# Kernel optimization log

Measured on AMD Instinct MI355X. Metric: run time of the kernel, lower is better.

The kernel has to match this reference:

```python
import jax, jax.numpy as jnp
import numpy as np

B, S, D = 2, 2048, 1024
H = 16
HD = D // H  # 64


def setup_inputs() -> dict:
    key = jax.random.key(0)
    k = jax.random.split(key, 6)
    s = 0.02
    return {
        "x": jax.random.normal(k[0], (B, S, D), dtype=jnp.float32),
        "wq": jax.random.normal(k[1], (D, D), dtype=jnp.float32) * s,
        "wk": jax.random.normal(k[2], (D, D), dtype=jnp.float32) * s,
        "wv": jax.random.normal(k[3], (D, D), dtype=jnp.float32) * s,
        "wo": jax.random.normal(k[4], (D, D), dtype=jnp.float32) * s,
        "bo": jnp.zeros((D,), dtype=jnp.float32),
    }


def reference(x, wq, wk, wv, wo, bo):
    b, n, d = x.shape
    # nn.Linear: y = x @ W.T (qkv_bias=False)
    def proj(w):
        y = jnp.einsum('bnd,od->bno', x, w)
        return y.reshape(b, n, H, HD).transpose(0, 2, 1, 3)  # (b, H, n, hd)
    q, k, v = proj(wq), proj(wk), proj(wv)
    scores = jnp.einsum('bhqd,bhkd->bhqk', q, k) / jnp.sqrt(jnp.float32(HD))
    # NOTE: source code slices the causal mask but never applies it; softmax is unmasked.
    attn = jax.nn.softmax(scores, axis=-1)
    # dropout p=0.0 -> identity
    ctx = jnp.einsum('bhqk,bhkd->bhqd', attn, v)
    ctx = ctx.transpose(0, 2, 1, 3).reshape(b, n, d)
    return jnp.einsum('bnd,od->bno', ctx, wo) + bo
```

## Files before the change

### kernel.cpp

```cpp
#include <hip/hip_runtime.h>
#include <hip/hip_bf16.h>
#include <stdint.h>

typedef __attribute__((ext_vector_type(8))) short short8;
typedef __attribute__((ext_vector_type(4))) float float4v;
typedef __attribute__((ext_vector_type(4))) unsigned short ushort4v;

#define Bq 2
#define Sq 2048
#define Dq 1024
#define Hq 16
#define HDq 64

#define QSCALE 0.18033688011112042f

__device__ __forceinline__ unsigned short f2bf(float f) {
  union { float f; uint32_t u; } v; v.f = f;
  uint32_t r = (v.u + 0x7FFFu + ((v.u >> 16) & 1u)) >> 16;
  return (unsigned short)r;
}

__device__ __forceinline__ uint32_t pk2bf(float a, float b) {
  union { __hip_bfloat162 h; uint32_t u; } cv;
  cv.h = __float22bfloat162_rn(make_float2(a, b));
  return cv.u;
}

__device__ __forceinline__ void gl_lds16(const unsigned short* g, unsigned short* l) {
  __builtin_amdgcn_global_load_lds(
      (const __attribute__((address_space(1))) void*)g,
      (__attribute__((address_space(3))) void*)l, 16, 0, 0);
}

__global__ __launch_bounds__(256) void cvt_all_kernel(
    const float* __restrict__ x,
    const float* __restrict__ w0, const float* __restrict__ w1,
    const float* __restrict__ w2, const float* __restrict__ w3,
    unsigned short* __restrict__ xb, unsigned short* __restrict__ wb) {
  const int bid = blockIdx.x;
  const float* src;
  unsigned short* dst;
  int idx;
  if (bid < 4096) {
    src = x; dst = xb;
    idx = bid * 256 + threadIdx.x;
  } else {
    int j = (bid - 4096) * 256 + threadIdx.x;
    int z = j >> 18;
    src = (z == 0) ? w0 : (z == 1) ? w1 : (z == 2) ? w2 : w3;
    dst = wb + (size_t)z * 1048576;
    idx = j & 262143;
  }
  float4v f = ((const float4v*)src)[idx];
  ushort4v o;
#pragma unroll
  for (int q = 0; q < 4; q++) o[q] = f2bf(f[q]);
  ((ushort4v*)dst)[idx] = o;
}

template <bool OUTPROJ, int MT>
__global__ __launch_bounds__(256) void gemm_bt_kernel(
    const unsigned short* __restrict__ A,
    const unsigned short* __restrict__ W0,
    const unsigned short* __restrict__ W1,
    const unsigned short* __restrict__ W2,
    unsigned short* __restrict__ q_dst,
    unsigned short* __restrict__ k_dst,
    unsigned short* __restrict__ v_dst,
    float* __restrict__ f_dst,
    const float* __restrict__ bias) {
  constexpr int K = 1024;
  constexpr int NMB = MT / 32;
  constexpr int APASS = MT / 32;
  const int z = blockIdx.z;
  const unsigned short* W = (z == 0) ? W0 : (z == 1) ? W1 : W2;
  unsigned short* qkv = (z == 0) ? q_dst : (z == 1) ? k_dst : v_dst;

  __shared__ unsigned short Asm[MT * 64];
  __shared__ unsigned short Bsm[128 * 64];

  const int t = threadIdx.x;
  const int wave = t >> 6, lane = t & 63;
  const int quad = lane >> 4, l16 = lane & 15;
  const int wy = wave >> 1, wx = wave & 1;
  const int row0 = blockIdx.x * MT;
  const int col0 = blockIdx.y * 128;

  float4v zero = {0.f, 0.f, 0.f, 0.f};
  float4v acc[NMB][4];
#pragma unroll
  for (int i = 0; i < NMB; i++)
#pragma unroll
    for (int j = 0; j < 4; j++) acc[i][j] = zero;

  const int srow = t >> 3;
  const int sgl = ((t & 7) ^ (srow & 7)) << 3;
  const unsigned short* gA[APASS];
  const unsigned short* gB[4];
#pragma unroll
  for (int i = 0; i < APASS; i++)
    gA[i] = A + (size_t)(row0 + i * 32 + srow) * K + sgl;
#pragma unroll
  for (int i = 0; i < 4; i++)
    gB[i] = W + (size_t)(col0 + i * 32 + srow) * K + sgl;

  const int swl = (l16 & 7);

  for (int k0 = 0; k0 < K; k0 += 64) {
#pragma unroll
    for (int i = 0; i < APASS; i++) gl_lds16(gA[i] + k0, &Asm[i * 2048 + t * 8]);
#pragma unroll
    for (int i = 0; i < 4; i++) gl_lds16(gB[i] + k0, &Bsm[i * 2048 + t * 8]);
    __syncthreads();
    short8 af[NMB][2], bf[4][2];
#pragma unroll
    for (int ks = 0; ks < 2; ks++) {
#pragma unroll
      for (int mb = 0; mb < NMB; mb++) {
        int row = wy * (MT / 2) + mb * 16 + l16;
        int pg = (ks * 4 + quad) ^ swl;
        af[mb][ks] = *(const short8*)(&Asm[row * 64 + pg * 8]);
      }
#pragma unroll
      for (int nb = 0; nb < 4; nb++) {
        int row = wx * 64 + nb * 16 + l16;
        int pg = (ks * 4 + quad) ^ swl;
        bf[nb][ks] = *(const short8*)(&Bsm[row * 64 + pg * 8]);
      }
    }
#pragma unroll
    for (int ks = 0; ks < 2; ks++)
#pragma unroll
      for (int mb = 0; mb < NMB; mb++)
#pragma unroll
        for (int nb = 0; nb < 4; nb++)
          acc[mb][nb] = __builtin_amdgcn_mfma_f32_16x16x32_bf16(af[mb][ks], bf[nb][ks], acc[mb][nb], 0, 0, 0);
    __syncthreads();
  }

  const float qsc = (!OUTPROJ && z == 0) ? QSCALE : 1.0f;
#pragma unroll
  for (int mb = 0; mb < NMB; mb++) {
#pragma unroll
    for (int nb = 0; nb < 4; nb++) {
#pragma unroll
      for (int r = 0; r < 4; r++) {
        int row = row0 + wy * (MT / 2) + mb * 16 + quad * 4 + r;
        int o = col0 + wx * 64 + nb * 16 + l16;
        float val = acc[mb][nb][r];
        if (OUTPROJ) {
          f_dst[(size_t)row * 1024 + o] = val + bias[o];
        } else {
          int b = row >> 11, s = row & 2047;
          int h = o >> 6, hd = o & 63;
          qkv[(size_t)((b * Hq + h) * Sq + s) * HDq + hd] = f2bf(val * qsc);
        }
      }
    }
  }
}

__global__ __launch_bounds__(512) void attn_kernel(
    const unsigned short* __restrict__ Q,
    const unsigned short* __restrict__ Kg,
    const unsigned short* __restrict__ Vg,
    unsigned short* __restrict__ ctx) {
  constexpr int KSTR = 68;
  constexpr int VSTR = 136;
  const int bh = blockIdx.y;
  const int q0 = blockIdx.x * 128;
  const int t = threadIdx.x;
  const int wave = t >> 6, lane = t & 63;
  const int quad = lane >> 4, l16 = lane & 15;

  __shared__ unsigned short Ksm[128 * KSTR];
  __shared__ unsigned short Vsm[64 * VSTR];

  const unsigned short* Qb = Q + (size_t)bh * Sq * HDq;
  const unsigned short* Kb = Kg + (size_t)bh * Sq * HDq;
  const unsigned short* Vb = Vg + (size_t)bh * Sq * HDq;

  short8 qf[2];
#pragma unroll
  for (int ks = 0; ks < 2; ks++)
    qf[ks] = *(const short8*)(Qb + (size_t)(q0 + wave * 16 + l16) * HDq + ks * 32 + quad * 8);

  short8 ones;
#pragma unroll
  for (int j = 0; j < 8; j++) ones[j] = (short)0x3F80;

  float4v zero = {0.f, 0.f, 0.f, 0.f};
  float4v of[4];
  float4v dsum = zero;
#pragma unroll
  for (int hb = 0; hb < 4; hb++) of[hb] = zero;

  const int kr0 = t >> 3, kc = (t & 7) << 3;
  const int vr2 = (t & 63) * 2;
  const int vc8 = (t >> 6) << 3;
  const int sig = (vr2 & ~31) + (((vr2 >> 2) & 3) << 3) + (((vr2 >> 4) & 1) << 2) + (vr2 & 3);

  short8 kpr[2], vpr0, vpr1;
#pragma unroll
  for (int i = 0; i < 2; i++)
    kpr[i] = *(const short8*)(Kb + (size_t)(kr0 + i * 64) * HDq + kc);
  vpr0 = *(const short8*)(Vb + (size_t)vr2 * HDq + vc8);
  vpr1 = *(const short8*)(Vb + (size_t)(vr2 + 1) * HDq + vc8);

  for (int kt = 0; kt < Sq; kt += 128) {
#pragma unroll
    for (int i = 0; i < 2; i++)
      *(short8*)(&Ksm[(kr0 + i * 64) * KSTR + kc]) = kpr[i];
#pragma unroll
    for (int j = 0; j < 8; j++) {
      uint32_t pk = (uint32_t)(unsigned short)vpr0[j] |
                    ((uint32_t)(unsigned short)vpr1[j] << 16);
      *(uint32_t*)(&Vsm[(vc8 + j) * VSTR + sig]) = pk;
    }
    __syncthreads();

    if (kt + 128 < Sq) {
      const unsigned short* Kn = Kb + (size_t)(kt + 128) * HDq;
      const unsigned short* Vn = Vb + (size_t)(kt + 128) * HDq;
#pragma unroll
      for (int i = 0; i < 2; i++)
        kpr[i] = *(const short8*)(Kn + (size_t)(kr0 + i * 64) * HDq + kc);
      vpr0 = *(const short8*)(Vn + (size_t)vr2 * HDq + vc8);
      vpr1 = *(const short8*)(Vn + (size_t)(vr2 + 1) * HDq + vc8);
    }

#pragma unroll
    for (int p = 0; p < 4; p++) {
      float4v sf[2] = {zero, zero};
#pragma unroll
      for (int s = 0; s < 2; s++)
#pragma unroll
        for (int ks = 0; ks < 2; ks++) {
          short8 kf = *(const short8*)(&Ksm[(p * 32 + s * 16 + l16) * KSTR + ks * 32 + quad * 8]);
          sf[s] = __builtin_amdgcn_mfma_f32_16x16x32_bf16(kf, qf[ks], sf[s], 0, 0, 0);
        }
      union { uint32_t u[4]; short8 v; } pw;
#pragma unroll
      for (int s = 0; s < 2; s++)
#pragma unroll
        for (int rp = 0; rp < 2; rp++) {
          float pa = __builtin_amdgcn_exp2f(sf[s][rp * 2]);
          float pb = __builtin_amdgcn_exp2f(sf[s][rp * 2 + 1]);
          pw.u[s * 2 + rp] = pk2bf(pa, pb);
        }
      short8 pf = pw.v;
      dsum = __builtin_amdgcn_mfma_f32_16x16x32_bf16(pf, ones, dsum, 0, 0, 0);
#pragma unroll
      for (int hb = 0; hb < 4; hb++) {
        short8 vf = *(const short8*)(&Vsm[(hb * 16 + l16) * VSTR + p * 32 + quad * 8]);
        of[hb] = __builtin_amdgcn_mfma_f32_16x16x32_bf16(pf, vf, of[hb], 0, 0, 0);
      }
    }
    __syncthreads();
  }

  const int b = bh >> 4, h = bh & 15;
  float4v dinv;
#pragma unroll
  for (int r = 0; r < 4; r++) dinv[r] = 1.0f / dsum[r];
#pragma unroll
  for (int hb = 0; hb < 4; hb++)
#pragma unroll
    for (int r = 0; r < 4; r++) {
      int srow = q0 + wave * 16 + quad * 4 + r;
      int d = h * 64 + hb * 16 + l16;
      ctx[(size_t)(b * Sq + srow) * Dq + d] = f2bf(of[hb][r] * dinv[r]);
    }
}

extern "C" void kernel_launch(void* const* d_in, const int* in_sizes, int n_in,
                              void* d_out, int out_size, void* d_ws, size_t ws_size,
                              hipStream_t stream) {
  (void)in_sizes; (void)n_in; (void)out_size; (void)ws_size;
  const float* x  = (const float*)d_in[0];
  const float* wq = (const float*)d_in[1];
  const float* wk = (const float*)d_in[2];
  const float* wv = (const float*)d_in[3];
  const float* wo = (const float*)d_in[4];
  const float* bo = (const float*)d_in[5];
  float* out = (float*)d_out;

  char* ws = (char*)d_ws;
  const size_t MB = 1u << 20;
  unsigned short* xb  = (unsigned short*)(ws + 0 * MB);
  unsigned short* wqb = (unsigned short*)(ws + 8 * MB);
  unsigned short* wkb = (unsigned short*)(ws + 10 * MB);
  unsigned short* wvb = (unsigned short*)(ws + 12 * MB);
  unsigned short* wob = (unsigned short*)(ws + 14 * MB);
  unsigned short* qb  = (unsigned short*)(ws + 16 * MB);
  unsigned short* kb  = (unsigned short*)(ws + 24 * MB);
  unsigned short* vb  = (unsigned short*)(ws + 32 * MB);
  unsigned short* cxb = (unsigned short*)(ws + 40 * MB);

  cvt_all_kernel<<<8192, 256, 0, stream>>>(x, wq, wk, wv, wo, xb, wqb);

  gemm_bt_kernel<false, 128><<<dim3(32, 8, 3), 256, 0, stream>>>(
      xb, wqb, wkb, wvb, qb, kb, vb, nullptr, nullptr);
  attn_kernel<<<dim3(16, 32), 512, 0, stream>>>(qb, kb, vb, cxb);
  gemm_bt_kernel<true, 64><<<dim3(64, 8, 1), 256, 0, stream>>>(
      cxb, wob, wob, wob, nullptr, nullptr, nullptr, out, bo);
}
```

Measured before the change: 185.6 us.

## Restructure attention into 4-wave split-K tiles with double-buffered LDS and async K loads

```diff
diff --git a/kernel.cpp b/kernel.cpp
--- a/kernel.cpp
+++ b/kernel.cpp
@@ -5,6 +5,7 @@
 typedef __attribute__((ext_vector_type(8))) short short8;
 typedef __attribute__((ext_vector_type(4))) float float4v;
 typedef __attribute__((ext_vector_type(4))) unsigned short ushort4v;
+typedef __attribute__((ext_vector_type(4))) unsigned int uint4v;
 
 #define Bq 2
 #define Sq 2048
@@ -160,117 +161,189 @@
   }
 }
 
-__global__ __launch_bounds__(512) void attn_kernel(
+__global__ __launch_bounds__(256) void attn_kernel(
     const unsigned short* __restrict__ Q,
     const unsigned short* __restrict__ Kg,
     const unsigned short* __restrict__ Vg,
     unsigned short* __restrict__ ctx) {
-  constexpr int KSTR = 68;
   constexpr int VSTR = 136;
+  constexpr int KBUF = 8192;
+  constexpr int VBUF = 8704;
+  __shared__ __align__(16) unsigned char smem[67584];
+  unsigned short* Ksm = (unsigned short*)smem;
+  unsigned short* Vsm = (unsigned short*)(smem + 32768);
+  float* obuf = (float*)smem;
+  float* dbuf = (float*)(smem + 34816);
+
   const int bh = blockIdx.y;
   const int q0 = blockIdx.x * 128;
   const int t = threadIdx.x;
   const int wave = t >> 6, lane = t & 63;
   const int quad = lane >> 4, l16 = lane & 15;
-
-  __shared__ unsigned short Ksm[128 * KSTR];
-  __shared__ unsigned short Vsm[64 * VSTR];
+  const int wq = wave >> 1, wk = wave & 1;
+  const int swl = l16 & 7;
 
   const unsigned short* Qb = Q + (size_t)bh * Sq * HDq;
   const unsigned short* Kb = Kg + (size_t)bh * Sq * HDq;
   const unsigned short* Vb = Vg + (size_t)bh * Sq * HDq;
 
-  short8 qf[2];
-#pragma unroll
-  for (int ks = 0; ks < 2; ks++)
-    qf[ks] = *(const short8*)(Qb + (size_t)(q0 + wave * 16 + l16) * HDq + ks * 32 + quad * 8);
+  short8 qf[4][2];
+#pragma unroll
+  for (int qb = 0; qb < 4; qb++)
+#pragma unroll
+    for (int ks = 0; ks < 2; ks++)
+      qf[qb][ks] = *(const short8*)(Qb + (size_t)(q0 + wq * 64 + qb * 16 + l16) * HDq + ks * 32 + quad * 8);
 
   short8 ones;
 #pragma unroll
   for (int j = 0; j < 8; j++) ones[j] = (short)0x3F80;
 
   float4v zero = {0.f, 0.f, 0.f, 0.f};
-  float4v of[4];
-  float4v dsum = zero;
-#pragma unroll
-  for (int hb = 0; hb < 4; hb++) of[hb] = zero;
-
-  const int kr0 = t >> 3, kc = (t & 7) << 3;
+  float4v of[4][4];
+  float4v dsum[4];
+#pragma unroll
+  for (int qb = 0; qb < 4; qb++) {
+    dsum[qb] = zero;
+#pragma unroll
+    for (int hb = 0; hb < 4; hb++) of[qb][hb] = zero;
+  }
+
+  const int srow = t >> 3;
+  const unsigned short* gK = Kb + (size_t)srow * 64 + (((t & 7) ^ (srow & 7)) << 3);
+
   const int vr2 = (t & 63) * 2;
-  const int vc8 = (t >> 6) << 3;
+  const int vc16 = (t >> 6) << 4;
   const int sig = (vr2 & ~31) + (((vr2 >> 2) & 3) << 3) + (((vr2 >> 4) & 1) << 2) + (vr2 & 3);
-
-  short8 kpr[2], vpr0, vpr1;
-#pragma unroll
-  for (int i = 0; i < 2; i++)
-    kpr[i] = *(const short8*)(Kb + (size_t)(kr0 + i * 64) * HDq + kc);
-  vpr0 = *(const short8*)(Vb + (size_t)vr2 * HDq + vc8);
-  vpr1 = *(const short8*)(Vb + (size_t)(vr2 + 1) * HDq + vc8);
+  const unsigned short* gV = Vb + (size_t)vr2 * 64 + vc16;
+
+  uint4v va0, va1, vb0, vb1;
+
+#define VLOAD(off) do {                                            \
+    const unsigned short* vp = gV + (size_t)(off) * 64;            \
+    va0 = *(const uint4v*)(vp);      vb0 = *(const uint4v*)(vp + 8); \
+    va1 = *(const uint4v*)(vp + 64); vb1 = *(const uint4v*)(vp + 72); \
+  } while (0)
+
+#define VPACK(bufsel) do {                                                   \
+    unsigned short* vd = &Vsm[(bufsel) * VBUF + sig];                        \
+    _Pragma("unroll")                                                        \
+    for (int r = 0; r < 4; r++) {                                            \
+      uint32_t w0 = __builtin_amdgcn_perm(va1[r], va0[r], 0x05040100u);      \
+      uint32_t w1 = __builtin_amdgcn_perm(va1[r], va0[r], 0x07060302u);      \
+      *(uint32_t*)(vd + (vc16 + 2 * r) * VSTR) = w0;                         \
+      *(uint32_t*)(vd + (vc16 + 2 * r + 1) * VSTR) = w1;                     \
+      uint32_t x0 = __builtin_amdgcn_perm(vb1[r], vb0[r], 0x05040100u);      \
+      uint32_t x1 = __builtin_amdgcn_perm(vb1[r], vb0[r], 0x07060302u);      \
+      *(uint32_t*)(vd + (vc16 + 8 + 2 * r) * VSTR) = x0;                     \
+      *(uint32_t*)(vd + (vc16 + 8 + 2 * r + 1) * VSTR) = x1;                 \
+    }                                                                        \
+  } while (0)
+
+#define KISSUE(off, bufsel) do {                                   \
+    _Pragma("unroll")                                              \
+    for (int i = 0; i < 4; i++)                                    \
+      gl_lds16(gK + (size_t)(off) * 64 + i * 2048,                 \
+               &Ksm[(bufsel) * KBUF + i * 2048 + t * 8]);          \
+  } while (0)
+
+  KISSUE(0, 0);
+  VLOAD(0);
+  VPACK(0);
+  VLOAD(128);
+  __syncthreads();
+  KISSUE(128, 1);
 
   for (int kt = 0; kt < Sq; kt += 128) {
-#pragma unroll
-    for (int i = 0; i < 2; i++)
-      *(short8*)(&Ksm[(kr0 + i * 64) * KSTR + kc]) = kpr[i];
-#pragma unroll
-    for (int j = 0; j < 8; j++) {
-      uint32_t pk = (uint32_t)(unsigned short)vpr0[j] |
-                    ((uint32_t)(unsigned short)vpr1[j] << 16);
-      *(uint32_t*)(&Vsm[(vc8 + j) * VSTR + sig]) = pk;
-    }
+    const int cur = (kt >> 7) & 1;
+#pragma unroll
+    for (int p = 0; p < 2; p++) {
+      const int kb0 = cur * KBUF + (wk * 64 + p * 32) * 64;
+      short8 kf[2][2];
+#pragma unroll
+      for (int s = 0; s < 2; s++)
+#pragma unroll
+        for (int ks = 0; ks < 2; ks++)
+          kf[s][ks] = *(const short8*)&Ksm[kb0 + (s * 16 + l16) * 64 + ((ks * 4 + quad) ^ swl) * 8];
+      short8 pf[4];
+#pragma unroll
+      for (int qb = 0; qb < 4; qb++) {
+        float4v s0 = zero, s1 = zero;
+#pragma unroll
+        for (int ks = 0; ks < 2; ks++) {
+          s0 = __builtin_amdgcn_mfma_f32_16x16x32_bf16(kf[0][ks], qf[qb][ks], s0, 0, 0, 0);
+          s1 = __builtin_amdgcn_mfma_f32_16x16x32_bf16(kf[1][ks], qf[qb][ks], s1, 0, 0, 0);
+        }
+        union { uint32_t u[4]; short8 v; } pw;
+        pw.u[0] = pk2bf(__builtin_amdgcn_exp2f(s0[0]), __builtin_amdgcn_exp2f(s0[1]));
+        pw.u[1] = pk2bf(__builtin_amdgcn_exp2f(s0[2]), __builtin_amdgcn_exp2f(s0[3]));
+        pw.u[2] = pk2bf(__builtin_amdgcn_exp2f(s1[0]), __builtin_amdgcn_exp2f(s1[1]));
+        pw.u[3] = pk2bf(__builtin_amdgcn_exp2f(s1[2]), __builtin_amdgcn_exp2f(s1[3]));
+        pf[qb] = pw.v;
+      }
+#pragma unroll
+      for (int qb = 0; qb < 4; qb++)
+        dsum[qb] = __builtin_amdgcn_mfma_f32_16x16x32_bf16(pf[qb], ones, dsum[qb], 0, 0, 0);
+      const int vbo = cur * VBUF + wk * 64 + p * 32 + quad * 8;
+#pragma unroll
+      for (int hb = 0; hb < 4; hb++) {
+        short8 vf = *(const short8*)&Vsm[vbo + (hb * 16 + l16) * VSTR];
+#pragma unroll
+        for (int qb = 0; qb < 4; qb++)
+          of[qb][hb] = __builtin_amdgcn_mfma_f32_16x16x32_bf16(pf[qb], vf, of[qb][hb], 0, 0, 0);
+      }
+    }
+    if (kt + 128 < Sq) VPACK(cur ^ 1);
+    if (kt + 256 < Sq) VLOAD(kt + 256);
     __syncthreads();
-
-    if (kt + 128 < Sq) {
-      const unsigned short* Kn = Kb + (size_t)(kt + 128) * HDq;
-      const unsigned short* Vn = Vb + (size_t)(kt + 128) * HDq;
-#pragma unroll
-      for (int i = 0; i < 2; i++)
-        kpr[i] = *(const short8*)(Kn + (size_t)(kr0 + i * 64) * HDq + kc);
-      vpr0 = *(const short8*)(Vn + (size_t)vr2 * HDq + vc8);
-      vpr1 = *(const short8*)(Vn + (size_t)(vr2 + 1) * HDq + vc8);
-    }
-
-#pragma unroll
-    for (int p = 0; p < 4; p++) {
-      float4v sf[2] = {zero, zero};
-#pragma unroll
-      for (int s = 0; s < 2; s++)
-#pragma unroll
-        for (int ks = 0; ks < 2; ks++) {
-          short8 kf = *(const short8*)(&Ksm[(p * 32 + s * 16 + l16) * KSTR + ks * 32 + quad * 8]);
-          sf[s] = __builtin_amdgcn_mfma_f32_16x16x32_bf16(kf, qf[ks], sf[s], 0, 0, 0);
-        }
-      union { uint32_t u[4]; short8 v; } pw;
-#pragma unroll
-      for (int s = 0; s < 2; s++)
-#pragma unroll
-        for (int rp = 0; rp < 2; rp++) {
-          float pa = __builtin_amdgcn_exp2f(sf[s][rp * 2]);
-          float pb = __builtin_amdgcn_exp2f(sf[s][rp * 2 + 1]);
-          pw.u[s * 2 + rp] = pk2bf(pa, pb);
-        }
-      short8 pf = pw.v;
-      dsum = __builtin_amdgcn_mfma_f32_16x16x32_bf16(pf, ones, dsum, 0, 0, 0);
+    if (kt + 256 < Sq) KISSUE(kt + 256, cur);
+  }
+
+  if (wk == 0) {
+#pragma unroll
+    for (int qb = 0; qb < 4; qb++) {
+#pragma unroll
+      for (int hb = 0; hb < 4; hb++)
+        *(float4v*)&obuf[(wq * 64 + hb * 16 + l16) * 68 + qb * 16 + quad * 4] = of[qb][hb];
+      if (l16 == 0)
+#pragma unroll
+        for (int r = 0; r < 4; r++)
+          dbuf[wq * 64 + qb * 16 + quad * 4 + r] = dsum[qb][r];
+    }
+  }
+  __syncthreads();
+  if (wk == 1) {
+#pragma unroll
+    for (int qb = 0; qb < 4; qb++) {
 #pragma unroll
       for (int hb = 0; hb < 4; hb++) {
-        short8 vf = *(const short8*)(&Vsm[(hb * 16 + l16) * VSTR + p * 32 + quad * 8]);
-        of[hb] = __builtin_amdgcn_mfma_f32_16x16x32_bf16(pf, vf, of[hb], 0, 0, 0);
-      }
-    }
-    __syncthreads();
-  }
+        float4v* pp = (float4v*)&obuf[(wq * 64 + hb * 16 + l16) * 68 + qb * 16 + quad * 4];
+        float4v o = *pp;
+        o += of[qb][hb];
+        *pp = o;
+      }
+      if (l16 == 0)
+#pragma unroll
+        for (int r = 0; r < 4; r++)
+          dbuf[wq * 64 + qb * 16 + quad * 4 + r] += dsum[qb][r];
+    }
+  }
+  __syncthreads();
 
   const int b = bh >> 4, h = bh & 15;
-  float4v dinv;
-#pragma unroll
-  for (int r = 0; r < 4; r++) dinv[r] = 1.0f / dsum[r];
-#pragma unroll
-  for (int hb = 0; hb < 4; hb++)
-#pragma unroll
-    for (int r = 0; r < 4; r++) {
-      int srow = q0 + wave * 16 + quad * 4 + r;
-      int d = h * 64 + hb * 16 + l16;
-      ctx[(size_t)(b * Sq + srow) * Dq + d] = f2bf(of[hb][r] * dinv[r]);
-    }
+  const int qq = t & 127, hseg = t >> 7;
+  const float dinv = 1.0f / dbuf[qq];
+  const float* ob = &obuf[(qq >> 6) * 4352 + (hseg * 32) * 68 + (qq & 63)];
+  unsigned short* cp = ctx + ((size_t)(b * Sq + q0 + qq)) * Dq + h * 64 + hseg * 32;
+#pragma unroll
+  for (int g = 0; g < 4; g++) {
+    short8 o8;
+#pragma unroll
+    for (int j = 0; j < 8; j++) o8[j] = (short)f2bf(ob[(g * 8 + j) * 68] * dinv);
+    *(short8*)(cp + g * 8) = o8;
+  }
+#undef VLOAD
+#undef VPACK
+#undef KISSUE
 }
 
 extern "C" void kernel_launch(void* const* d_in, const int* in_sizes, int n_in,
@@ -301,7 +374,7 @@
 
   gemm_bt_kernel<false, 128><<<dim3(32, 8, 3), 256, 0, stream>>>(
       xb, wqb, wkb, wvb, qb, kb, vb, nullptr, nullptr);
-  attn_kernel<<<dim3(16, 32), 512, 0, stream>>>(qb, kb, vb, cxb);
+  attn_kernel<<<dim3(16, 32), 256, 0, stream>>>(qb, kb, vb, cxb);
   gemm_bt_kernel<true, 64><<<dim3(64, 8, 1), 256, 0, stream>>>(
       cxb, wob, wob, wob, nullptr, nullptr, nullptr, out, bo);
 }
```

After: 192.8 us. 1.04x slower.
